# Kernel optimization log

Measured on AMD Instinct MI355X. Metric: run time of the kernel, lower is better.

## Reference

```python
import jax, jax.numpy as jnp
import numpy as np


def setup_inputs() -> dict:
    key = jax.random.key(0)
    k1, k2, k3, k4 = jax.random.split(key, 4)
    B, T, M, Din, Dout = 32, 24, 512, 64, 64
    x = jax.random.normal(k1, (B, T, M, Din), dtype=jnp.float32)
    adj = jax.random.uniform(k2, (M, M), dtype=jnp.float32)
    adj = adj / jnp.sum(adj, axis=-1, keepdims=True)  # row-normalized adjacency
    route_weights = jax.random.normal(k3, (M, Din, Dout), dtype=jnp.float32) * 0.05
    route_bias = jax.random.normal(k4, (M, 1, Dout), dtype=jnp.float32) * 0.05
    return {"x": x, "adj": adj, "route_weights": route_weights, "route_bias": route_bias}


def reference(x, adj, route_weights, route_bias):
    B, T, M, _ = x.shape
    xf = x.reshape(B * T, M, -1)                      # [BT, M, Din]
    # shared adjacency applied across all B*T graphs: one contraction instead of
    # a broadcast bmm
    h = jnp.einsum('mn,bnd->bmd', adj, xf)            # [BT, M, Din]
    # per-node (per-route) weight transform + per-route bias
    h = jnp.einsum('bmd,mdl->bml', h, route_weights)  # [BT, M, Dout]
    h = h + route_bias[:, 0, :][None, :, :]           # bias per route m
    return h.reshape(B, T, M, -1)
```

## Files before the change

kernel.cpp:

```cpp
#include <hip/hip_runtime.h>
#include <stdint.h>

typedef short bf16x8 __attribute__((ext_vector_type(8)));
typedef unsigned short u16x8 __attribute__((ext_vector_type(8)));
typedef float f32x4 __attribute__((ext_vector_type(4)));
typedef float f32x8 __attribute__((ext_vector_type(8)));

constexpr int BT_TOT = 768;
constexpr int M_N    = 512;
constexpr int DD     = 64;
constexpr int WROW   = 72;

__device__ __forceinline__ unsigned short f2bf(float f) {
  unsigned u = __builtin_bit_cast(unsigned, f);
  u += 0x7fffu + ((u >> 16) & 1u);
  return (unsigned short)(u >> 16);
}

__global__ __launch_bounds__(256)
void prep_adj(const float* __restrict__ adjg, unsigned short* __restrict__ wsadj) {
  int i = (blockIdx.x * 256 + threadIdx.x) * 8;
  f32x8 a = *(const f32x8*)(adjg + i);
  u16x8 r;
  #pragma unroll
  for (int j = 0; j < 8; ++j) r[j] = f2bf(a[j]);
  *(u16x8*)(wsadj + i) = r;
}

template<bool WS>
__global__ __launch_bounds__(256, 2)
void gconv_h(const float* __restrict__ xg,
             const float* __restrict__ adjf,
             const unsigned short* __restrict__ adjb,
             char* __restrict__ hout)
{
  __shared__ unsigned short xT[64 * 512];

  const int bt   = blockIdx.x;
  const int tid  = threadIdx.x;
  const int lane = tid & 63;
  const int wv   = tid >> 6;
  const int l15  = lane & 15;
  const int gg   = lane >> 4;
  const int nq   = tid & 31;
  const int doct = tid >> 5;

  const float* xb = xg + (size_t)bt * (M_N * DD);

  f32x8 x0, x1, x2, x3;
  { const float* p = xb + (nq*4)*DD + doct*8;
    x0 = *(const f32x8*)p;        x1 = *(const f32x8*)(p+DD);
    x2 = *(const f32x8*)(p+2*DD); x3 = *(const f32x8*)(p+3*DD); }
  #pragma unroll
  for (int c = 0; c < 4; ++c) {
    #pragma unroll
    for (int e = 0; e < 8; ++e) {
      int d = doct*8 + e;
      unsigned v0 = (unsigned)f2bf(x0[e]) | ((unsigned)f2bf(x1[e]) << 16);
      unsigned v1 = (unsigned)f2bf(x2[e]) | ((unsigned)f2bf(x3[e]) << 16);
      uint2 vv; vv.x = v0; vv.y = v1;
      *(uint2*)(&xT[d*512 + (((c*16) + (nq>>1)) ^ e)*8 + (nq&1)*4]) = vv;
    }
    if (c < 3) {
      const float* p = xb + ((c+1)*128 + nq*4)*DD + doct*8;
      x0 = *(const f32x8*)p;        x1 = *(const f32x8*)(p+DD);
      x2 = *(const f32x8*)(p+2*DD); x3 = *(const f32x8*)(p+3*DD);
    }
  }
  __syncthreads();

  f32x4 acc[8][4];
  #pragma unroll
  for (int mt = 0; mt < 8; ++mt)
    #pragma unroll
    for (int dt = 0; dt < 4; ++dt) acc[mt][dt] = f32x4{0.f,0.f,0.f,0.f};

  #pragma unroll 2
  for (int kl = 0; kl < 16; ++kl) {
    bf16x8 afr[8];
    #pragma unroll
    for (int mt = 0; mt < 8; ++mt) {
      const int m = wv*128 + mt*16 + l15;
      if (WS) {
        afr[mt] = __builtin_bit_cast(bf16x8,
            *(const u16x8*)(adjb + (size_t)m*M_N + kl*32 + gg*8));
      } else {
        f32x8 a = *(const f32x8*)(adjf + (size_t)m*M_N + kl*32 + gg*8);
        u16x8 r;
        #pragma unroll
        for (int j = 0; j < 8; ++j) r[j] = f2bf(a[j]);
        afr[mt] = __builtin_bit_cast(bf16x8, r);
      }
    }
    #pragma unroll
    for (int dt = 0; dt < 4; ++dt) {
      const int d = dt*16 + l15;
      bf16x8 bfx = __builtin_bit_cast(bf16x8,
          *(const u16x8*)(&xT[d*512 + ((kl*4 + gg) ^ (l15 & 7))*8]));
      #pragma unroll
      for (int mt = 0; mt < 8; ++mt)
        acc[mt][dt] = __builtin_amdgcn_mfma_f32_16x16x32_bf16(afr[mt], bfx,
                                                              acc[mt][dt], 0,0,0);
    }
  }

  #pragma unroll
  for (int mt = 0; mt < 8; ++mt)
    #pragma unroll
    for (int dt = 0; dt < 4; ++dt)
      #pragma unroll
      for (int r = 0; r < 4; ++r) {
        int m = wv*128 + mt*16 + gg*4 + r;
        int d = dt*16 + l15;
        *(unsigned short*)(hout + ((size_t)bt*M_N + m)*256 + 2*d)
            = f2bf(acc[mt][dt][r]);
      }
}

__global__ __launch_bounds__(256, 4)
void route_mm(const char* __restrict__ hin,
              const float* __restrict__ wgt,
              const float* __restrict__ bias,
              float* __restrict__ outg)
{
  __shared__ unsigned short wb[128 * WROW];

  const int m0    = blockIdx.x * 2;
  const int btblk = blockIdx.y * 64;
  const int tid   = threadIdx.x;
  const int lane  = tid & 63;
  const int wv    = tid >> 6;
  const int l15   = lane & 15;
  const int gg    = lane >> 4;
  const int dp    = tid & 31;
  const int lo    = tid >> 5;

  { const float* q = wgt + ((size_t)m0*64 + dp*2)*64 + lo*8;
    f32x8 w0 = *(const f32x8*)q;          f32x8 w1 = *(const f32x8*)(q+64);
    f32x8 w2 = *(const f32x8*)(q+4096);   f32x8 w3 = *(const f32x8*)(q+4160);
    #pragma unroll
    for (int e = 0; e < 8; ++e) {
      int lrow = lo*8 + e;
      unsigned v0 = (unsigned)f2bf(w0[e]) | ((unsigned)f2bf(w1[e]) << 16);
      unsigned v1 = (unsigned)f2bf(w2[e]) | ((unsigned)f2bf(w3[e]) << 16);
      *(unsigned*)(wb + lrow*WROW + dp*2)        = v0;
      *(unsigned*)(wb + (64 + lrow)*WROW + dp*2) = v1;
    }
  }
  __syncthreads();

  const int btw0 = btblk + wv*16;

  #pragma unroll
  for (int mm = 0; mm < 2; ++mm) {
    const int m = m0 + mm;
    bf16x8 afr[2];
    #pragma unroll
    for (int ks = 0; ks < 2; ++ks) {
      const char* hp = hin + ((size_t)(btw0 + l15)*M_N + m)*256 + ks*64 + gg*16;
      afr[ks] = __builtin_bit_cast(bf16x8, *(const u16x8*)hp);
    }
    f32x4 acc[4];
    #pragma unroll
    for (int lt = 0; lt < 4; ++lt) acc[lt] = f32x4{0.f,0.f,0.f,0.f};
    #pragma unroll
    for (int lt = 0; lt < 4; ++lt)
      #pragma unroll
      for (int ks = 0; ks < 2; ++ks) {
        bf16x8 bfr = __builtin_bit_cast(bf16x8,
            *(const u16x8*)(wb + (mm*64 + lt*16 + l15)*WROW + ks*32 + gg*8));
        acc[lt] = __builtin_amdgcn_mfma_f32_16x16x32_bf16(afr[ks], bfr, acc[lt], 0,0,0);
      }
    #pragma unroll
    for (int lt = 0; lt < 4; ++lt) {
      float bv = bias[m*64 + lt*16 + l15];
      #pragma unroll
      for (int r = 0; r < 4; ++r) {
        size_t row = (size_t)(btw0 + gg*4 + r)*M_N + m;
        outg[row*64 + lt*16 + l15] = acc[lt][r] + bv;
      }
    }
  }
}

extern "C" void kernel_launch(void* const* d_in, const int* in_sizes, int n_in,
                              void* d_out, int out_size, void* d_ws, size_t ws_size,
                              hipStream_t stream) {
  const float* xg   = (const float*)d_in[0];
  const float* adjg = (const float*)d_in[1];
  const float* wgt  = (const float*)d_in[2];
  const float* bg   = (const float*)d_in[3];

  const size_t adj_bf_bytes = (size_t)M_N * M_N * 2;
  if (ws_size >= adj_bf_bytes) {
    unsigned short* wsadj = (unsigned short*)d_ws;
    prep_adj<<<dim3(M_N * M_N / (256 * 8)), dim3(256), 0, stream>>>(adjg, wsadj);
    gconv_h<true><<<dim3(BT_TOT), dim3(256), 0, stream>>>(
        xg, adjg, wsadj, (char*)d_out);
  } else {
    gconv_h<false><<<dim3(BT_TOT), dim3(256), 0, stream>>>(
        xg, adjg, nullptr, (char*)d_out);
  }
  route_mm<<<dim3(M_N/2, BT_TOT/64), dim3(256), 0, stream>>>(
      (const char*)d_out, wgt, bg, (float*)d_out);
}
```

Measured before the change: 105.6 us.

## Chunk x staging into double-buffered LDS and double gconv block size

```diff
diff --git a/kernel.cpp b/kernel.cpp
--- a/kernel.cpp
+++ b/kernel.cpp
@@ -28,13 +28,13 @@
 }
 
 template<bool WS>
-__global__ __launch_bounds__(256, 2)
+__global__ __launch_bounds__(512, 4)
 void gconv_h(const float* __restrict__ xg,
              const float* __restrict__ adjf,
              const unsigned short* __restrict__ adjb,
              char* __restrict__ hout)
 {
-  __shared__ unsigned short xT[64 * 512];
+  __shared__ unsigned short xTc[2][64 * 128];
 
   const int bt   = blockIdx.x;
   const int tid  = threadIdx.x;
@@ -42,75 +42,74 @@
   const int wv   = tid >> 6;
   const int l15  = lane & 15;
   const int gg   = lane >> 4;
-  const int nq   = tid & 31;
-  const int doct = tid >> 5;
+  const int nd   = tid & 63;
+  const int dct  = tid >> 6;
 
   const float* xb = xg + (size_t)bt * (M_N * DD);
 
-  f32x8 x0, x1, x2, x3;
-  { const float* p = xb + (nq*4)*DD + doct*8;
-    x0 = *(const f32x8*)p;        x1 = *(const f32x8*)(p+DD);
-    x2 = *(const f32x8*)(p+2*DD); x3 = *(const f32x8*)(p+3*DD); }
+  f32x8 x0, x1;
+  { const float* p = xb + (nd*2)*DD + dct*8;
+    x0 = *(const f32x8*)p;  x1 = *(const f32x8*)(p + DD); }
+
+  f32x4 acc[4][4];
+  #pragma unroll
+  for (int mt = 0; mt < 4; ++mt)
+    #pragma unroll
+    for (int dt = 0; dt < 4; ++dt) acc[mt][dt] = f32x4{0.f,0.f,0.f,0.f};
+
   #pragma unroll
   for (int c = 0; c < 4; ++c) {
+    unsigned short* xt = &xTc[c & 1][0];
     #pragma unroll
     for (int e = 0; e < 8; ++e) {
-      int d = doct*8 + e;
-      unsigned v0 = (unsigned)f2bf(x0[e]) | ((unsigned)f2bf(x1[e]) << 16);
-      unsigned v1 = (unsigned)f2bf(x2[e]) | ((unsigned)f2bf(x3[e]) << 16);
-      uint2 vv; vv.x = v0; vv.y = v1;
-      *(uint2*)(&xT[d*512 + (((c*16) + (nq>>1)) ^ e)*8 + (nq&1)*4]) = vv;
+      int d = dct*8 + e;
+      unsigned v = (unsigned)f2bf(x0[e]) | ((unsigned)f2bf(x1[e]) << 16);
+      *(unsigned*)(xt + d*128 + (((nd>>2) ^ e) * 8) + (nd&3)*2) = v;
     }
     if (c < 3) {
-      const float* p = xb + ((c+1)*128 + nq*4)*DD + doct*8;
-      x0 = *(const f32x8*)p;        x1 = *(const f32x8*)(p+DD);
-      x2 = *(const f32x8*)(p+2*DD); x3 = *(const f32x8*)(p+3*DD);
-    }
-  }
-  __syncthreads();
-
-  f32x4 acc[8][4];
-  #pragma unroll
-  for (int mt = 0; mt < 8; ++mt)
-    #pragma unroll
-    for (int dt = 0; dt < 4; ++dt) acc[mt][dt] = f32x4{0.f,0.f,0.f,0.f};
-
-  #pragma unroll 2
-  for (int kl = 0; kl < 16; ++kl) {
-    bf16x8 afr[8];
-    #pragma unroll
-    for (int mt = 0; mt < 8; ++mt) {
-      const int m = wv*128 + mt*16 + l15;
-      if (WS) {
-        afr[mt] = __builtin_bit_cast(bf16x8,
-            *(const u16x8*)(adjb + (size_t)m*M_N + kl*32 + gg*8));
-      } else {
-        f32x8 a = *(const f32x8*)(adjf + (size_t)m*M_N + kl*32 + gg*8);
-        u16x8 r;
+      const float* p = xb + ((c+1)*128 + nd*2)*DD + dct*8;
+      x0 = *(const f32x8*)p;  x1 = *(const f32x8*)(p + DD);
+    }
+    __syncthreads();
+
+    #pragma unroll
+    for (int kl = 0; kl < 4; ++kl) {
+      const int kg = c*4 + kl;
+      bf16x8 afr[4];
+      #pragma unroll
+      for (int mt = 0; mt < 4; ++mt) {
+        const int m = wv*64 + mt*16 + l15;
+        if (WS) {
+          afr[mt] = __builtin_bit_cast(bf16x8,
+              *(const u16x8*)(adjb + (size_t)m*M_N + kg*32 + gg*8));
+        } else {
+          f32x8 a = *(const f32x8*)(adjf + (size_t)m*M_N + kg*32 + gg*8);
+          u16x8 r;
+          #pragma unroll
+          for (int j = 0; j < 8; ++j) r[j] = f2bf(a[j]);
+          afr[mt] = __builtin_bit_cast(bf16x8, r);
+        }
+      }
+      #pragma unroll
+      for (int dt = 0; dt < 4; ++dt) {
+        const int d = dt*16 + l15;
+        bf16x8 bfx = __builtin_bit_cast(bf16x8,
+            *(const u16x8*)(xt + d*128 + (((kl*4 + gg) ^ (l15 & 7)))*8));
         #pragma unroll
-        for (int j = 0; j < 8; ++j) r[j] = f2bf(a[j]);
-        afr[mt] = __builtin_bit_cast(bf16x8, r);
-      }
-    }
-    #pragma unroll
-    for (int dt = 0; dt < 4; ++dt) {
-      const int d = dt*16 + l15;
-      bf16x8 bfx = __builtin_bit_cast(bf16x8,
-          *(const u16x8*)(&xT[d*512 + ((kl*4 + gg) ^ (l15 & 7))*8]));
-      #pragma unroll
-      for (int mt = 0; mt < 8; ++mt)
-        acc[mt][dt] = __builtin_amdgcn_mfma_f32_16x16x32_bf16(afr[mt], bfx,
-                                                              acc[mt][dt], 0,0,0);
-    }
-  }
-
-  #pragma unroll
-  for (int mt = 0; mt < 8; ++mt)
+        for (int mt = 0; mt < 4; ++mt)
+          acc[mt][dt] = __builtin_amdgcn_mfma_f32_16x16x32_bf16(afr[mt], bfx,
+                                                                acc[mt][dt], 0,0,0);
+      }
+    }
+  }
+
+  #pragma unroll
+  for (int mt = 0; mt < 4; ++mt)
     #pragma unroll
     for (int dt = 0; dt < 4; ++dt)
       #pragma unroll
       for (int r = 0; r < 4; ++r) {
-        int m = wv*128 + mt*16 + gg*4 + r;
+        int m = wv*64 + mt*16 + gg*4 + r;
         int d = dt*16 + l15;
         *(unsigned short*)(hout + ((size_t)bt*M_N + m)*256 + 2*d)
             = f2bf(acc[mt][dt][r]);
@@ -195,10 +194,10 @@
   if (ws_size >= adj_bf_bytes) {
     unsigned short* wsadj = (unsigned short*)d_ws;
     prep_adj<<<dim3(M_N * M_N / (256 * 8)), dim3(256), 0, stream>>>(adjg, wsadj);
-    gconv_h<true><<<dim3(BT_TOT), dim3(256), 0, stream>>>(
+    gconv_h<true><<<dim3(BT_TOT), dim3(512), 0, stream>>>(
         xg, adjg, wsadj, (char*)d_out);
   } else {
-    gconv_h<false><<<dim3(BT_TOT), dim3(256), 0, stream>>>(
+    gconv_h<false><<<dim3(BT_TOT), dim3(512), 0, stream>>>(
         xg, adjg, nullptr, (char*)d_out);
   }
   route_mm<<<dim3(M_N/2, BT_TOT/64), dim3(256), 0, stream>>>(
```

Result: slower. 124.7 us (+18.0%).
